# Kernel optimization log

Measured on AMD Instinct MI355X. Metric: run time of the kernel, lower is better.

The kernel has to match this reference:

```python
import jax, jax.numpy as jnp
import numpy as np

B, S, D = 1, 2048, 4096
H, KV = 32, 8
HD = D // H  # 128
NEG = -1e9


def _rope(t, cos, sin):
    # t: [B,S,h,HD]; cos/sin: [S,HD//2] -> broadcast [1,S,1,HD//2]
    tr = t[..., 0::2]
    ti = t[..., 1::2]
    c = cos[None, :, None, :]
    s = sin[None, :, None, :]
    out_r = tr * c - ti * s
    out_i = tr * s + ti * c
    # interleave back: (..., HD//2, 2) -> (..., HD)
    return jnp.stack([out_r, out_i], axis=-1).reshape(t.shape)


def setup_inputs() -> dict:
    key = jax.random.key(0)
    ks = jax.random.split(key, 5)
    w_scale = 0.02
    x = jax.random.normal(ks[0], (B, S, D), dtype=jnp.float32)
    wq = jax.random.normal(ks[1], (H * HD, D), dtype=jnp.float32) * w_scale
    wk = jax.random.normal(ks[2], (KV * HD, D), dtype=jnp.float32) * w_scale
    wv = jax.random.normal(ks[3], (KV * HD, D), dtype=jnp.float32) * w_scale
    wo = jax.random.normal(ks[4], (D, H * HD), dtype=jnp.float32) * w_scale
    # RoPE tables (theta = 10000)
    inv_freq = 1.0 / (10000.0 ** (np.arange(0, HD, 2, dtype=np.float32) / HD))
    angles = np.arange(S, dtype=np.float32)[:, None] * inv_freq[None, :]  # [S, HD//2]
    freqs_cos = jnp.asarray(np.cos(angles))
    freqs_sin = jnp.asarray(np.sin(angles))
    # causal additive mask [1,1,S,S]
    causal = jnp.tril(jnp.ones((S, S), dtype=bool))
    mask = jnp.where(causal, 0.0, NEG).astype(jnp.float32)[None, None]
    return {"x": x, "wq": wq, "wk": wk, "wv": wv, "wo": wo,
            "freqs_cos": freqs_cos, "freqs_sin": freqs_sin, "mask": mask}


def reference(x, wq, wk, wv, wo, freqs_cos, freqs_sin, mask):
    b, s, d = x.shape
    q = (x @ wq.T).reshape(b, s, H, HD)
    k = (x @ wk.T).reshape(b, s, KV, HD)
    v = (x @ wv.T).reshape(b, s, KV, HD)
    q = _rope(q, freqs_cos, freqs_sin)
    k = _rope(k, freqs_cos, freqs_sin)
    rep = H // KV
    k = jnp.repeat(k, rep, axis=2)  # [b,s,H,HD]
    v = jnp.repeat(v, rep, axis=2)
    scores = jnp.einsum('bshd,bthd->bhst', q, k) / jnp.sqrt(jnp.float32(HD))
    scores = scores + mask
    attn = jax.nn.softmax(scores, axis=-1)
    out = jnp.einsum('bhst,bthd->bshd', attn, v).reshape(b, s, H * HD)
    return out @ wo.T
```

## Files before the change

kernel.cpp:

```cpp
#include <hip/hip_runtime.h>
#include <hip/hip_bf16.h>
#include <math.h>

#define SEQ 2048
#define DIM 4096
#define NH 32
#define NKV 8
#define HD 128
#define KVD 1024
#define SCALE 0.08838834764831845f
#define NEGBIG -1000000000.0f

typedef __bf16 bf16;
typedef __attribute__((ext_vector_type(2))) __bf16 bf16x2;
typedef __attribute__((ext_vector_type(4))) __bf16 bf16x4;
typedef __attribute__((ext_vector_type(8))) __bf16 bf16x8;
typedef __attribute__((ext_vector_type(4))) float f32x4;

__device__ __forceinline__ void async_g2l16(const bf16* g, bf16* l) {
  __builtin_amdgcn_global_load_lds(
      (const __attribute__((address_space(1))) void*)g,
      (__attribute__((address_space(3))) void*)l,
      16, 0, 0);
}

#define SEG_X  2097152
#define SEG_WQ 4194304
#define SEG_WK 1048576
#define C0 SEG_X
#define C1 (C0 + SEG_WQ)
#define C2 (C1 + SEG_WK)
#define C3 (C2 + SEG_WK)
#define C4 (C3 + SEG_WQ)

__global__ void cast_all_kernel(const float* __restrict__ x,
                                const float* __restrict__ wq,
                                const float* __restrict__ wk,
                                const float* __restrict__ wv,
                                const float* __restrict__ wo,
                                bf16* __restrict__ xb, bf16* __restrict__ wqb,
                                bf16* __restrict__ wkb, bf16* __restrict__ wvb,
                                bf16* __restrict__ wob) {
  int i = blockIdx.x * 256 + threadIdx.x;
  const float* src; bf16* dst; int j;
  if (i < C0)      { src = x;  dst = xb;  j = i; }
  else if (i < C1) { src = wq; dst = wqb; j = i - C0; }
  else if (i < C2) { src = wk; dst = wkb; j = i - C1; }
  else if (i < C3) { src = wv; dst = wvb; j = i - C2; }
  else             { src = wo; dst = wob; j = i - C3; }
  float4 v = ((const float4*)src)[j];
  bf16x4 o;
  o[0] = (bf16)v.x; o[1] = (bf16)v.y; o[2] = (bf16)v.z; o[3] = (bf16)v.w;
  ((bf16x4*)dst)[j] = o;
}

__device__ __forceinline__ void gemm_core(
    const bf16* __restrict__ A, int lda,
    const bf16* __restrict__ B, int ldb,
    int K, int mBase, f32x4 acc[4][4])
{
  __shared__ __align__(16) bf16 As[128 * 32];
  __shared__ __align__(16) bf16 Bs[128 * 32];

  const int tid  = threadIdx.x;
  const int lane = tid & 63;
  const int w    = tid >> 6;
  const int l15  = lane & 15;
  const int quad = lane >> 4;
  const int wr   = (w >> 1) * 64;
  const int wc   = (w & 1) * 64;

  const int srow = lane >> 2;
  const int kswz = ((lane & 3) ^ ((srow >> 1) & 3)) * 8;
  const bf16* gA0 = A + (size_t)(mBase + w * 16 + srow) * lda + kswz;
  const bf16* gA1 = gA0 + (size_t)64 * lda;
  const bf16* gB0 = B + (size_t)(w * 16 + srow) * ldb + kswz;
  const bf16* gB1 = gB0 + (size_t)64 * ldb;
  bf16* lA0 = As + w * 512;
  bf16* lA1 = As + (w + 4) * 512;
  bf16* lB0 = Bs + w * 512;
  bf16* lB1 = Bs + (w + 4) * 512;

  const f32x4 vzero = {0.f, 0.f, 0.f, 0.f};
#pragma unroll
  for (int mi = 0; mi < 4; ++mi)
#pragma unroll
    for (int ni = 0; ni < 4; ++ni) acc[mi][ni] = vzero;

  const int rsw = ((l15 >> 1) & 3);

  for (int k0 = 0; k0 < K; k0 += 32) {
    __syncthreads();
    async_g2l16(gA0 + k0, lA0);
    async_g2l16(gA1 + k0, lA1);
    async_g2l16(gB0 + k0, lB0);
    async_g2l16(gB1 + k0, lB1);
    __syncthreads();

    bf16x8 a[4], b[4];
#pragma unroll
    for (int mi = 0; mi < 4; ++mi)
      a[mi] = *(const bf16x8*)(As + (wr + mi * 16 + l15) * 32 +
                               ((quad ^ rsw) * 8));
#pragma unroll
    for (int ni = 0; ni < 4; ++ni)
      b[ni] = *(const bf16x8*)(Bs + (wc + ni * 16 + l15) * 32 +
                               ((quad ^ rsw) * 8));
#pragma unroll
    for (int mi = 0; mi < 4; ++mi)
#pragma unroll
      for (int ni = 0; ni < 4; ++ni)
        acc[mi][ni] = __builtin_amdgcn_mfma_f32_16x16x32_bf16(
            a[mi], b[ni], acc[mi][ni], 0, 0, 0);
  }
}

__global__ __launch_bounds__(256, 2) void qkv_gemm_kernel(
    const bf16* __restrict__ xb, const bf16* __restrict__ wqb,
    const bf16* __restrict__ wkb, const bf16* __restrict__ wvb,
    const float* __restrict__ fc, const float* __restrict__ fs,
    bf16* __restrict__ Qb, bf16* __restrict__ Kb, bf16* __restrict__ Vt)
{
  const int nb = blockIdx.x;
  const int mBase = blockIdx.y * 128;
  const bf16* Bm;
  if (nb < 32)      Bm = wqb + (size_t)nb * 128 * DIM;
  else if (nb < 40) Bm = wkb + (size_t)(nb - 32) * 128 * DIM;
  else              Bm = wvb + (size_t)(nb - 40) * 128 * DIM;

  f32x4 acc[4][4];
  gemm_core(xb, DIM, Bm, DIM, DIM, mBase, acc);

  const int tid  = threadIdx.x;
  const int lane = tid & 63;
  const int w    = tid >> 6;
  const int l15  = lane & 15;
  const int quad = lane >> 4;
  const int wr   = (w >> 1) * 64;
  const int wc   = (w & 1) * 64;

  if (nb < 40) {
    const bool isQ = (nb < 32);
    bf16* dst = isQ ? (Qb + nb * HD) : (Kb + (nb - 32) * HD);
    const int ldd = isQ ? DIM : KVD;
    const float sc = isQ ? SCALE : 1.0f;
    const int odd = l15 & 1;
#pragma unroll
    for (int mi = 0; mi < 4; ++mi) {
#pragma unroll
      for (int ni = 0; ni < 4; ++ni) {
        int d = wc + ni * 16 + l15;
        int fidx = d >> 1;
#pragma unroll
        for (int r = 0; r < 4; ++r) {
          int s = mBase + wr + mi * 16 + quad * 4 + r;
          float v  = acc[mi][ni][r];
          float pv = __shfl_xor(v, 1, 64);
          float c  = fc[s * 64 + fidx];
          float sn = fs[s * 64 + fidx];
          float o  = odd ? (pv * sn + v * c) : (v * c - pv * sn);
          dst[(size_t)s * ldd + d] = (bf16)(o * sc);
        }
      }
    }
  } else {
    const int t = nb - 40;
#pragma unroll
    for (int mi = 0; mi < 4; ++mi) {
      int srow = mBase + wr + mi * 16 + quad * 4;
#pragma unroll
      for (int ni = 0; ni < 4; ++ni) {
        int d = wc + ni * 16 + l15;
        bf16x4 pv;
#pragma unroll
        for (int r = 0; r < 4; ++r) pv[r] = (bf16)acc[mi][ni][r];
        *(bf16x4*)(Vt + ((size_t)t * HD + d) * SEQ + srow) = pv;
      }
    }
  }
}

__global__ __launch_bounds__(256, 2) void out_gemm_kernel(
    const bf16* __restrict__ attnb, const bf16* __restrict__ wob,
    float* __restrict__ out)
{
  const int mBase = blockIdx.y * 128;
  f32x4 acc[4][4];
  gemm_core(attnb, DIM, wob + (size_t)blockIdx.x * 128 * DIM, DIM, DIM,
            mBase, acc);

  const int tid  = threadIdx.x;
  const int lane = tid & 63;
  const int w    = tid >> 6;
  const int l15  = lane & 15;
  const int quad = lane >> 4;
  const int wr   = (w >> 1) * 64;
  const int wc   = (w & 1) * 64;
#pragma unroll
  for (int mi = 0; mi < 4; ++mi) {
    int row = mBase + wr + mi * 16 + quad * 4;
#pragma unroll
    for (int ni = 0; ni < 4; ++ni) {
      int col = blockIdx.x * 128 + wc + ni * 16 + l15;
#pragma unroll
      for (int r = 0; r < 4; ++r)
        out[(size_t)(row + r) * DIM + col] = acc[mi][ni][r];
    }
  }
}

__global__ __launch_bounds__(256, 2) void attn_kernel(
    const bf16* __restrict__ Qb, const bf16* __restrict__ Kb,
    const bf16* __restrict__ Vt, bf16* __restrict__ attnb)
{
  __shared__ __align__(16) bf16 Ks[64 * 128];
  __shared__ __align__(16) bf16 Vs[128 * 64];
  __shared__ __align__(16) bf16 Ps[128 * 64];

  const int b    = blockIdx.x;
  const int half = b >> 8;
  const int r8   = b & 255;
  const int h    = (half << 4) | (r8 >> 4);
  const int qt   = half ? (r8 & 15) : 15 - (r8 & 15);
  const int kvh  = h >> 2;
  const int qbase = qt * 128;

  const int tid  = threadIdx.x;
  const int lane = tid & 63;
  const int w    = tid >> 6;
  const int l15  = lane & 15;
  const int quad = lane >> 4;

  bf16x8 qfrag[2][4];
#pragma unroll
  for (int n = 0; n < 2; ++n) {
    int q = qbase + w * 32 + n * 16 + l15;
#pragma unroll
    for (int ks = 0; ks < 4; ++ks)
      qfrag[n][ks] = *(const bf16x8*)(Qb + (size_t)q * DIM + h * HD +
                                      ks * 32 + quad * 8);
  }

  const f32x4 vzero = {0.f, 0.f, 0.f, 0.f};
  f32x4 oacc[8][2];
#pragma unroll
  for (int dm = 0; dm < 8; ++dm)
#pragma unroll
    for (int n = 0; n < 2; ++n) oacc[dm][n] = vzero;
  float m_run[2] = {-1e30f, -1e30f};
  float l_run[2] = {0.f, 0.f};

  const int nkt = 2 * (qt + 1);
  for (int kt = 0; kt < nkt; ++kt) {
    const int kbase = kt * 64;

    __syncthreads();
#pragma unroll
    for (int t = 0; t < 4; ++t) {
      int kr0 = w * 16 + t * 4;
      int krow = kr0 + (lane >> 4);
      int kg = (lane & 15) ^ (krow & 7);
      async_g2l16(Kb + (size_t)(kbase + krow) * KVD + kvh * HD + kg * 8,
                  Ks + kr0 * 128);
      int vr0 = w * 32 + t * 8;
      int d = vr0 + (lane >> 3);
      int vg = (lane & 7) ^ (d & 7);
      async_g2l16(Vt + ((size_t)kvh * HD + d) * SEQ + kbase + vg * 8,
                  Vs + vr0 * 64);
    }
    __syncthreads();

    f32x4 sacc[4][2];
#pragma unroll
    for (int kg = 0; kg < 4; ++kg)
#pragma unroll
      for (int n = 0; n < 2; ++n) sacc[kg][n] = vzero;
#pragma unroll
    for (int kg = 0; kg < 4; ++kg) {
      bf16x8 kf[4];
#pragma unroll
      for (int ks = 0; ks < 4; ++ks) {
        int row = kg * 16 + l15;
        kf[ks] = *(const bf16x8*)(Ks + row * 128 +
                                  (((ks * 4 + quad) ^ (row & 7)) * 8));
      }
#pragma unroll
      for (int n = 0; n < 2; ++n)
#pragma unroll
        for (int ks = 0; ks < 4; ++ks)
          sacc[kg][n] = __builtin_amdgcn_mfma_f32_16x16x32_bf16(
              kf[ks], qfrag[n][ks], sacc[kg][n], 0, 0, 0);
    }

#pragma unroll
    for (int n = 0; n < 2; ++n) {
      const int qloc = w * 32 + n * 16 + l15;
      const int qglob = qbase + qloc;
      if (kbase + 63 > qbase + w * 32 + n * 16) {
#pragma unroll
        for (int kg = 0; kg < 4; ++kg)
#pragma unroll
          for (int r = 0; r < 4; ++r) {
            int key = kbase + kg * 16 + quad * 4 + r;
            if (key > qglob) sacc[kg][n][r] = NEGBIG;
          }
      }
      float mx = -1e30f;
#pragma unroll
      for (int kg = 0; kg < 4; ++kg)
#pragma unroll
        for (int r = 0; r < 4; ++r) mx = fmaxf(mx, sacc[kg][n][r]);
      mx = fmaxf(mx, __shfl_xor(mx, 16, 64));
      mx = fmaxf(mx, __shfl_xor(mx, 32, 64));
      float mnew = fmaxf(m_run[n], mx);
      float alpha = __expf(m_run[n] - mnew);
      m_run[n] = mnew;
      float rs = 0.f;
#pragma unroll
      for (int kg = 0; kg < 4; ++kg) {
        bf16x4 pk;
#pragma unroll
        for (int r = 0; r < 4; ++r) {
          float p = __expf(sacc[kg][n][r] - mnew);
          rs += p;
          pk[r] = (bf16)p;
        }
        int g16 = (kg * 2 + (quad >> 1)) ^ (qloc & 7);
        *(bf16x4*)(Ps + qloc * 64 + g16 * 8 + (quad & 1) * 4) = pk;
      }
      rs += __shfl_xor(rs, 16, 64);
      rs += __shfl_xor(rs, 32, 64);
      l_run[n] = alpha * l_run[n] + rs;
#pragma unroll
      for (int dm = 0; dm < 8; ++dm)
#pragma unroll
        for (int r = 0; r < 4; ++r) oacc[dm][n][r] *= alpha;
    }

    bf16x8 pf[2][2];
#pragma unroll
    for (int kk = 0; kk < 2; ++kk)
#pragma unroll
      for (int n = 0; n < 2; ++n) {
        int qloc = w * 32 + n * 16 + l15;
        pf[kk][n] = *(const bf16x8*)(Ps + qloc * 64 +
                                     (((kk * 4 + quad) ^ (qloc & 7)) * 8));
      }
#pragma unroll
    for (int dm = 0; dm < 8; ++dm) {
#pragma unroll
      for (int kk = 0; kk < 2; ++kk) {
        int d = dm * 16 + l15;
        bf16x8 vf = *(const bf16x8*)(Vs + d * 64 +
                                     (((kk * 4 + quad) ^ (d & 7)) * 8));
#pragma unroll
        for (int n = 0; n < 2; ++n)
          oacc[dm][n] = __builtin_amdgcn_mfma_f32_16x16x32_bf16(
              vf, pf[kk][n], oacc[dm][n], 0, 0, 0);
      }
    }
  }

#pragma unroll
  for (int n = 0; n < 2; ++n) {
    float inv = 1.0f / l_run[n];
    int q = qbase + w * 32 + n * 16 + l15;
#pragma unroll
    for (int dm = 0; dm < 8; ++dm) {
      bf16x4 ov;
#pragma unroll
      for (int r = 0; r < 4; ++r) ov[r] = (bf16)(oacc[dm][n][r] * inv);
      *(bf16x4*)(attnb + (size_t)q * DIM + h * HD + dm * 16 + quad * 4) = ov;
    }
  }
}

extern "C" void kernel_launch(void* const* d_in, const int* in_sizes, int n_in,
                              void* d_out, int out_size, void* d_ws, size_t ws_size,
                              hipStream_t stream) {
  const float* x  = (const float*)d_in[0];
  const float* wq = (const float*)d_in[1];
  const float* wk = (const float*)d_in[2];
  const float* wv = (const float*)d_in[3];
  const float* wo = (const float*)d_in[4];
  const float* fc = (const float*)d_in[5];
  const float* fs = (const float*)d_in[6];
  float* out = (float*)d_out;

  size_t off = 0;
  char* wsb = (char*)d_ws;
  auto take = [&](size_t bytes) -> void* {
    void* p = wsb + off;
    off += (bytes + 255) & ~(size_t)255;
    return p;
  };
  bf16*  xb    = (bf16*)take((size_t)SEQ * DIM * 2);
  bf16*  wqb   = (bf16*)take((size_t)DIM * DIM * 2);
  bf16*  wkb   = (bf16*)take((size_t)KVD * DIM * 2);
  bf16*  wvb   = (bf16*)take((size_t)KVD * DIM * 2);
  bf16*  wob   = (bf16*)take((size_t)DIM * DIM * 2);
  bf16*  Qb    = (bf16*)take((size_t)SEQ * DIM * 2);
  bf16*  Kb    = (bf16*)take((size_t)SEQ * KVD * 2);
  bf16*  Vt    = (bf16*)take((size_t)NKV * HD * SEQ * 2);
  bf16*  attnb = (bf16*)take((size_t)SEQ * DIM * 2);

  cast_all_kernel<<<C4 / 256, 256, 0, stream>>>(x, wq, wk, wv, wo,
                                                xb, wqb, wkb, wvb, wob);

  qkv_gemm_kernel<<<dim3(48, 16), 256, 0, stream>>>(xb, wqb, wkb, wvb,
                                                    fc, fs, Qb, Kb, Vt);

  attn_kernel<<<dim3(512), 256, 0, stream>>>(Qb, Kb, Vt, attnb);

  out_gemm_kernel<<<dim3(32, 16), 256, 0, stream>>>(attnb, wob, out);
}
```

Before: 483.1 us.

## Fuse fp32-to-bf16 casting into GEMM tile loads and drop cast kernel

Removes the standalone cast kernel and has the QKV and output GEMMs load fp32 activations and weights directly into shared memory via async global-to-LDS copies, converting to bf16 when fragments are read from LDS. This removes a full pass that wrote and re-read bf16 copies of all weights and the input. In exchange, each GEMM tile load moves twice the bytes, LDS footprint grows, and conversion instructions are added inside the inner loop, which may reduce occupancy or stall the MFMA pipeline.

```diff
diff --git a/kernel.cpp b/kernel.cpp
--- a/kernel.cpp
+++ b/kernel.cpp
@@ -17,50 +17,22 @@
 typedef __attribute__((ext_vector_type(8))) __bf16 bf16x8;
 typedef __attribute__((ext_vector_type(4))) float f32x4;
 
-__device__ __forceinline__ void async_g2l16(const bf16* g, bf16* l) {
+__device__ __forceinline__ void async_g2l16(const void* g, void* l) {
   __builtin_amdgcn_global_load_lds(
       (const __attribute__((address_space(1))) void*)g,
       (__attribute__((address_space(3))) void*)l,
       16, 0, 0);
 }
 
-#define SEG_X  2097152
-#define SEG_WQ 4194304
-#define SEG_WK 1048576
-#define C0 SEG_X
-#define C1 (C0 + SEG_WQ)
-#define C2 (C1 + SEG_WK)
-#define C3 (C2 + SEG_WK)
-#define C4 (C3 + SEG_WQ)
-
-__global__ void cast_all_kernel(const float* __restrict__ x,
-                                const float* __restrict__ wq,
-                                const float* __restrict__ wk,
-                                const float* __restrict__ wv,
-                                const float* __restrict__ wo,
-                                bf16* __restrict__ xb, bf16* __restrict__ wqb,
-                                bf16* __restrict__ wkb, bf16* __restrict__ wvb,
-                                bf16* __restrict__ wob) {
-  int i = blockIdx.x * 256 + threadIdx.x;
-  const float* src; bf16* dst; int j;
-  if (i < C0)      { src = x;  dst = xb;  j = i; }
-  else if (i < C1) { src = wq; dst = wqb; j = i - C0; }
-  else if (i < C2) { src = wk; dst = wkb; j = i - C1; }
-  else if (i < C3) { src = wv; dst = wvb; j = i - C2; }
-  else             { src = wo; dst = wob; j = i - C3; }
-  float4 v = ((const float4*)src)[j];
-  bf16x4 o;
-  o[0] = (bf16)v.x; o[1] = (bf16)v.y; o[2] = (bf16)v.z; o[3] = (bf16)v.w;
-  ((bf16x4*)dst)[j] = o;
-}
-
+template<typename TA>
 __device__ __forceinline__ void gemm_core(
-    const bf16* __restrict__ A, int lda,
-    const bf16* __restrict__ B, int ldb,
+    const TA* __restrict__ A, int lda,
+    const float* __restrict__ B, int ldb,
     int K, int mBase, f32x4 acc[4][4])
 {
-  __shared__ __align__(16) bf16 As[128 * 32];
-  __shared__ __align__(16) bf16 Bs[128 * 32];
+  constexpr bool AF32 = (sizeof(TA) == 4);
+  __shared__ __align__(16) TA    As[128 * 32];
+  __shared__ __align__(16) float Bs[128 * 32];
 
   const int tid  = threadIdx.x;
   const int lane = tid & 63;
@@ -70,16 +42,11 @@
   const int wr   = (w >> 1) * 64;
   const int wc   = (w & 1) * 64;
 
+  const int r8 = lane >> 3;
+  const int gsw = (lane & 7) ^ r8;
+
   const int srow = lane >> 2;
   const int kswz = ((lane & 3) ^ ((srow >> 1) & 3)) * 8;
-  const bf16* gA0 = A + (size_t)(mBase + w * 16 + srow) * lda + kswz;
-  const bf16* gA1 = gA0 + (size_t)64 * lda;
-  const bf16* gB0 = B + (size_t)(w * 16 + srow) * ldb + kswz;
-  const bf16* gB1 = gB0 + (size_t)64 * ldb;
-  bf16* lA0 = As + w * 512;
-  bf16* lA1 = As + (w + 4) * 512;
-  bf16* lB0 = Bs + w * 512;
-  bf16* lB1 = Bs + (w + 4) * 512;
 
   const f32x4 vzero = {0.f, 0.f, 0.f, 0.f};
 #pragma unroll
@@ -91,21 +58,56 @@
 
   for (int k0 = 0; k0 < K; k0 += 32) {
     __syncthreads();
-    async_g2l16(gA0 + k0, lA0);
-    async_g2l16(gA1 + k0, lA1);
-    async_g2l16(gB0 + k0, lB0);
-    async_g2l16(gB1 + k0, lB1);
+    if constexpr (AF32) {
+#pragma unroll
+      for (int t = 0; t < 4; ++t) {
+        int row = w * 32 + t * 8 + r8;
+        async_g2l16((const float*)A + (size_t)(mBase + row) * lda + k0 + gsw * 4,
+                    As + (w * 32 + t * 8) * 32);
+      }
+    } else {
+      async_g2l16((const bf16*)A + (size_t)(mBase + w * 16 + srow) * lda + k0 + kswz,
+                  As + w * 512);
+      async_g2l16((const bf16*)A + (size_t)(mBase + 64 + w * 16 + srow) * lda + k0 + kswz,
+                  As + (w + 4) * 512);
+    }
+#pragma unroll
+    for (int t = 0; t < 4; ++t) {
+      int row = w * 32 + t * 8 + r8;
+      async_g2l16(B + (size_t)row * ldb + k0 + gsw * 4,
+                  Bs + (w * 32 + t * 8) * 32);
+    }
     __syncthreads();
 
     bf16x8 a[4], b[4];
 #pragma unroll
-    for (int mi = 0; mi < 4; ++mi)
-      a[mi] = *(const bf16x8*)(As + (wr + mi * 16 + l15) * 32 +
-                               ((quad ^ rsw) * 8));
-#pragma unroll
-    for (int ni = 0; ni < 4; ++ni)
-      b[ni] = *(const bf16x8*)(Bs + (wc + ni * 16 + l15) * 32 +
-                               ((quad ^ rsw) * 8));
+    for (int mi = 0; mi < 4; ++mi) {
+      int row = wr + mi * 16 + l15;
+      if constexpr (AF32) {
+        const float* rp = (const float*)As + row * 32;
+        int p0 = (2 * quad) ^ (row & 7);
+        f32x4 lo = *(const f32x4*)(rp + p0 * 4);
+        f32x4 hi = *(const f32x4*)(rp + (p0 ^ 1) * 4);
+        bf16x8 f;
+#pragma unroll
+        for (int j = 0; j < 4; ++j) { f[j] = (bf16)lo[j]; f[4 + j] = (bf16)hi[j]; }
+        a[mi] = f;
+      } else {
+        a[mi] = *(const bf16x8*)((const bf16*)As + row * 32 + ((quad ^ rsw) * 8));
+      }
+    }
+#pragma unroll
+    for (int ni = 0; ni < 4; ++ni) {
+      int row = wc + ni * 16 + l15;
+      const float* rp = Bs + row * 32;
+      int p0 = (2 * quad) ^ (row & 7);
+      f32x4 lo = *(const f32x4*)(rp + p0 * 4);
+      f32x4 hi = *(const f32x4*)(rp + (p0 ^ 1) * 4);
+      bf16x8 f;
+#pragma unroll
+      for (int j = 0; j < 4; ++j) { f[j] = (bf16)lo[j]; f[4 + j] = (bf16)hi[j]; }
+      b[ni] = f;
+    }
 #pragma unroll
     for (int mi = 0; mi < 4; ++mi)
 #pragma unroll
@@ -116,20 +118,20 @@
 }
 
 __global__ __launch_bounds__(256, 2) void qkv_gemm_kernel(
-    const bf16* __restrict__ xb, const bf16* __restrict__ wqb,
-    const bf16* __restrict__ wkb, const bf16* __restrict__ wvb,
+    const float* __restrict__ x, const float* __restrict__ wq,
+    const float* __restrict__ wk, const float* __restrict__ wv,
     const float* __restrict__ fc, const float* __restrict__ fs,
     bf16* __restrict__ Qb, bf16* __restrict__ Kb, bf16* __restrict__ Vt)
 {
   const int nb = blockIdx.x;
   const int mBase = blockIdx.y * 128;
-  const bf16* Bm;
-  if (nb < 32)      Bm = wqb + (size_t)nb * 128 * DIM;
-  else if (nb < 40) Bm = wkb + (size_t)(nb - 32) * 128 * DIM;
-  else              Bm = wvb + (size_t)(nb - 40) * 128 * DIM;
+  const float* Bm;
+  if (nb < 32)      Bm = wq + (size_t)nb * 128 * DIM;
+  else if (nb < 40) Bm = wk + (size_t)(nb - 32) * 128 * DIM;
+  else              Bm = wv + (size_t)(nb - 40) * 128 * DIM;
 
   f32x4 acc[4][4];
-  gemm_core(xb, DIM, Bm, DIM, DIM, mBase, acc);
+  gemm_core<float>(x, DIM, Bm, DIM, DIM, mBase, acc);
 
   const int tid  = threadIdx.x;
   const int lane = tid & 63;
@@ -181,13 +183,13 @@
 }
 
 __global__ __launch_bounds__(256, 2) void out_gemm_kernel(
-    const bf16* __restrict__ attnb, const bf16* __restrict__ wob,
+    const bf16* __restrict__ attnb, const float* __restrict__ wo,
     float* __restrict__ out)
 {
   const int mBase = blockIdx.y * 128;
   f32x4 acc[4][4];
-  gemm_core(attnb, DIM, wob + (size_t)blockIdx.x * 128 * DIM, DIM, DIM,
-            mBase, acc);
+  gemm_core<bf16>(attnb, DIM, wo + (size_t)blockIdx.x * 128 * DIM, DIM, DIM,
+                  mBase, acc);
 
   const int tid  = threadIdx.x;
   const int lane = tid & 63;
@@ -394,23 +396,15 @@
     off += (bytes + 255) & ~(size_t)255;
     return p;
   };
-  bf16*  xb    = (bf16*)take((size_t)SEQ * DIM * 2);
-  bf16*  wqb   = (bf16*)take((size_t)DIM * DIM * 2);
-  bf16*  wkb   = (bf16*)take((size_t)KVD * DIM * 2);
-  bf16*  wvb   = (bf16*)take((size_t)KVD * DIM * 2);
-  bf16*  wob   = (bf16*)take((size_t)DIM * DIM * 2);
   bf16*  Qb    = (bf16*)take((size_t)SEQ * DIM * 2);
   bf16*  Kb    = (bf16*)take((size_t)SEQ * KVD * 2);
   bf16*  Vt    = (bf16*)take((size_t)NKV * HD * SEQ * 2);
   bf16*  attnb = (bf16*)take((size_t)SEQ * DIM * 2);
 
-  cast_all_kernel<<<C4 / 256, 256, 0, stream>>>(x, wq, wk, wv, wo,
-                                                xb, wqb, wkb, wvb, wob);
-
-  qkv_gemm_kernel<<<dim3(48, 16), 256, 0, stream>>>(xb, wqb, wkb, wvb,
+  qkv_gemm_kernel<<<dim3(48, 16), 256, 0, stream>>>(x, wq, wk, wv,
                                                     fc, fs, Qb, Kb, Vt);
 
   attn_kernel<<<dim3(512), 256, 0, stream>>>(Qb, Kb, Vt, attnb);
 
-  out_gemm_kernel<<<dim3(32, 16), 256, 0, stream>>>(attnb, wob, out);
-}
+  out_gemm_kernel<<<dim3(32, 16), 256, 0, stream>>>(attnb, wo, out);
+}
```

Measured after the change: 573.6 us. +18.7%, slower.

## Shrink attention query tile to 64 rows and double grid size

Applied to the files above, without the earlier changes.

The attention kernel now gives each block 64 query rows instead of 128, with each wave owning 16 rows, and launches 1024 blocks instead of 512. Causal masking is applied only on the diagonal key tile, and the P buffer in shared memory is halved. Launch bounds rise to 3 blocks per CU. The aim is more parallelism, better load balance across CUs and higher occupancy through fewer registers per thread. In exchange, each K/V tile loaded into shared memory is reused by half as many queries, so K/V traffic roughly doubles.

```diff
diff --git a/kernel.cpp b/kernel.cpp
--- a/kernel.cpp
+++ b/kernel.cpp
@@ -17,7 +17,7 @@
 typedef __attribute__((ext_vector_type(8))) __bf16 bf16x8;
 typedef __attribute__((ext_vector_type(4))) float f32x4;
 
-__device__ __forceinline__ void async_g2l16(const bf16* g, bf16* l) {
+__device__ __forceinline__ void async_g2l16(const void* g, void* l) {
   __builtin_amdgcn_global_load_lds(
       (const __attribute__((address_space(1))) void*)g,
       (__attribute__((address_space(3))) void*)l,
@@ -209,48 +209,43 @@
   }
 }
 
-__global__ __launch_bounds__(256, 2) void attn_kernel(
+__global__ __launch_bounds__(256, 3) void attn_kernel(
     const bf16* __restrict__ Qb, const bf16* __restrict__ Kb,
     const bf16* __restrict__ Vt, bf16* __restrict__ attnb)
 {
   __shared__ __align__(16) bf16 Ks[64 * 128];
   __shared__ __align__(16) bf16 Vs[128 * 64];
-  __shared__ __align__(16) bf16 Ps[128 * 64];
+  __shared__ __align__(16) bf16 Ps[64 * 64];
 
   const int b    = blockIdx.x;
-  const int half = b >> 8;
-  const int r8   = b & 255;
-  const int h    = (half << 4) | (r8 >> 4);
-  const int qt   = half ? (r8 & 15) : 15 - (r8 & 15);
+  const int half = b >> 9;
+  const int r    = b & 511;
+  const int h    = (half << 4) | (r >> 5);
+  const int qt   = half ? (r & 31) : 31 - (r & 31);
   const int kvh  = h >> 2;
-  const int qbase = qt * 128;
+  const int qbase = qt * 64;
 
   const int tid  = threadIdx.x;
   const int lane = tid & 63;
   const int w    = tid >> 6;
   const int l15  = lane & 15;
   const int quad = lane >> 4;
-
-  bf16x8 qfrag[2][4];
-#pragma unroll
-  for (int n = 0; n < 2; ++n) {
-    int q = qbase + w * 32 + n * 16 + l15;
-#pragma unroll
-    for (int ks = 0; ks < 4; ++ks)
-      qfrag[n][ks] = *(const bf16x8*)(Qb + (size_t)q * DIM + h * HD +
-                                      ks * 32 + quad * 8);
-  }
+  const int qloc = w * 16 + l15;
+  const int qglob = qbase + qloc;
+
+  bf16x8 qfrag[4];
+#pragma unroll
+  for (int ks = 0; ks < 4; ++ks)
+    qfrag[ks] = *(const bf16x8*)(Qb + (size_t)qglob * DIM + h * HD +
+                                 ks * 32 + quad * 8);
 
   const f32x4 vzero = {0.f, 0.f, 0.f, 0.f};
-  f32x4 oacc[8][2];
-#pragma unroll
-  for (int dm = 0; dm < 8; ++dm)
-#pragma unroll
-    for (int n = 0; n < 2; ++n) oacc[dm][n] = vzero;
-  float m_run[2] = {-1e30f, -1e30f};
-  float l_run[2] = {0.f, 0.f};
-
-  const int nkt = 2 * (qt + 1);
+  f32x4 oacc[8];
+#pragma unroll
+  for (int dm = 0; dm < 8; ++dm) oacc[dm] = vzero;
+  float m_run = -1e30f, l_run = 0.f;
+
+  const int nkt = qt + 1;
   for (int kt = 0; kt < nkt; ++kt) {
     const int kbase = kt * 64;
 
@@ -270,11 +265,9 @@
     }
     __syncthreads();
 
-    f32x4 sacc[4][2];
-#pragma unroll
-    for (int kg = 0; kg < 4; ++kg)
-#pragma unroll
-      for (int n = 0; n < 2; ++n) sacc[kg][n] = vzero;
+    f32x4 sacc[4];
+#pragma unroll
+    for (int kg = 0; kg < 4; ++kg) sacc[kg] = vzero;
 #pragma unroll
     for (int kg = 0; kg < 4; ++kg) {
       bf16x8 kf[4];
@@ -285,67 +278,57 @@
                                   (((ks * 4 + quad) ^ (row & 7)) * 8));
       }
 #pragma unroll
-      for (int n = 0; n < 2; ++n)
-#pragma unroll
-        for (int ks = 0; ks < 4; ++ks)
-          sacc[kg][n] = __builtin_amdgcn_mfma_f32_16x16x32_bf16(
-              kf[ks], qfrag[n][ks], sacc[kg][n], 0, 0, 0);
-    }
-
-#pragma unroll
-    for (int n = 0; n < 2; ++n) {
-      const int qloc = w * 32 + n * 16 + l15;
-      const int qglob = qbase + qloc;
-      if (kbase + 63 > qbase + w * 32 + n * 16) {
-#pragma unroll
-        for (int kg = 0; kg < 4; ++kg)
-#pragma unroll
-          for (int r = 0; r < 4; ++r) {
-            int key = kbase + kg * 16 + quad * 4 + r;
-            if (key > qglob) sacc[kg][n][r] = NEGBIG;
-          }
-      }
-      float mx = -1e30f;
+      for (int ks = 0; ks < 4; ++ks)
+        sacc[kg] = __builtin_amdgcn_mfma_f32_16x16x32_bf16(
+            kf[ks], qfrag[ks], sacc[kg], 0, 0, 0);
+    }
+
+    if (kt == qt) {
 #pragma unroll
       for (int kg = 0; kg < 4; ++kg)
 #pragma unroll
-        for (int r = 0; r < 4; ++r) mx = fmaxf(mx, sacc[kg][n][r]);
-      mx = fmaxf(mx, __shfl_xor(mx, 16, 64));
-      mx = fmaxf(mx, __shfl_xor(mx, 32, 64));
-      float mnew = fmaxf(m_run[n], mx);
-      float alpha = __expf(m_run[n] - mnew);
-      m_run[n] = mnew;
-      float rs = 0.f;
-#pragma unroll
-      for (int kg = 0; kg < 4; ++kg) {
-        bf16x4 pk;
-#pragma unroll
         for (int r = 0; r < 4; ++r) {
-          float p = __expf(sacc[kg][n][r] - mnew);
-          rs += p;
-          pk[r] = (bf16)p;
+          int key = kbase + kg * 16 + quad * 4 + r;
+          if (key > qglob) sacc[kg][r] = NEGBIG;
         }
-        int g16 = (kg * 2 + (quad >> 1)) ^ (qloc & 7);
-        *(bf16x4*)(Ps + qloc * 64 + g16 * 8 + (quad & 1) * 4) = pk;
-      }
-      rs += __shfl_xor(rs, 16, 64);
-      rs += __shfl_xor(rs, 32, 64);
-      l_run[n] = alpha * l_run[n] + rs;
-#pragma unroll
-      for (int dm = 0; dm < 8; ++dm)
-#pragma unroll
-        for (int r = 0; r < 4; ++r) oacc[dm][n][r] *= alpha;
-    }
-
-    bf16x8 pf[2][2];
+    }
+
+    float mx = -1e30f;
+#pragma unroll
+    for (int kg = 0; kg < 4; ++kg)
+#pragma unroll
+      for (int r = 0; r < 4; ++r) mx = fmaxf(mx, sacc[kg][r]);
+    mx = fmaxf(mx, __shfl_xor(mx, 16, 64));
+    mx = fmaxf(mx, __shfl_xor(mx, 32, 64));
+    float mnew = fmaxf(m_run, mx);
+    float alpha = __expf(m_run - mnew);
+    m_run = mnew;
+    float rs = 0.f;
+#pragma unroll
+    for (int kg = 0; kg < 4; ++kg) {
+      bf16x4 pk;
+#pragma unroll
+      for (int r = 0; r < 4; ++r) {
+        float p = __expf(sacc[kg][r] - mnew);
+        rs += p;
+        pk[r] = (bf16)p;
+      }
+      int g16 = (kg * 2 + (quad >> 1)) ^ (qloc & 7);
+      *(bf16x4*)(Ps + qloc * 64 + g16 * 8 + (quad & 1) * 4) = pk;
+    }
+    rs += __shfl_xor(rs, 16, 64);
+    rs += __shfl_xor(rs, 32, 64);
+    l_run = alpha * l_run + rs;
+#pragma unroll
+    for (int dm = 0; dm < 8; ++dm)
+#pragma unroll
+      for (int r = 0; r < 4; ++r) oacc[dm][r] *= alpha;
+
+    bf16x8 pf[2];
 #pragma unroll
     for (int kk = 0; kk < 2; ++kk)
-#pragma unroll
-      for (int n = 0; n < 2; ++n) {
-        int qloc = w * 32 + n * 16 + l15;
-        pf[kk][n] = *(const bf16x8*)(Ps + qloc * 64 +
-                                     (((kk * 4 + quad) ^ (qloc & 7)) * 8));
-      }
+      pf[kk] = *(const bf16x8*)(Ps + qloc * 64 +
+                                (((kk * 4 + quad) ^ (qloc & 7)) * 8));
 #pragma unroll
     for (int dm = 0; dm < 8; ++dm) {
 #pragma unroll
@@ -353,24 +336,20 @@
         int d = dm * 16 + l15;
         bf16x8 vf = *(const bf16x8*)(Vs + d * 64 +
                                      (((kk * 4 + quad) ^ (d & 7)) * 8));
-#pragma unroll
-        for (int n = 0; n < 2; ++n)
-          oacc[dm][n] = __builtin_amdgcn_mfma_f32_16x16x32_bf16(
-              vf, pf[kk][n], oacc[dm][n], 0, 0, 0);
-      }
-    }
-  }
-
-#pragma unroll
-  for (int n = 0; n < 2; ++n) {
-    float inv = 1.0f / l_run[n];
-    int q = qbase + w * 32 + n * 16 + l15;
+        oacc[dm] = __builtin_amdgcn_mfma_f32_16x16x32_bf16(
+            vf, pf[kk], oacc[dm], 0, 0, 0);
+      }
+    }
+  }
+
+  {
+    float inv = 1.0f / l_run;
 #pragma unroll
     for (int dm = 0; dm < 8; ++dm) {
       bf16x4 ov;
 #pragma unroll
-      for (int r = 0; r < 4; ++r) ov[r] = (bf16)(oacc[dm][n][r] * inv);
-      *(bf16x4*)(attnb + (size_t)q * DIM + h * HD + dm * 16 + quad * 4) = ov;
+      for (int r = 0; r < 4; ++r) ov[r] = (bf16)(oacc[dm][r] * inv);
+      *(bf16x4*)(attnb + (size_t)qglob * DIM + h * HD + dm * 16 + quad * 4) = ov;
     }
   }
 }
@@ -410,7 +389,7 @@
   qkv_gemm_kernel<<<dim3(48, 16), 256, 0, stream>>>(xb, wqb, wkb, wvb,
                                                     fc, fs, Qb, Kb, Vt);
 
-  attn_kernel<<<dim3(512), 256, 0, stream>>>(Qb, Kb, Vt, attnb);
+  attn_kernel<<<dim3(1024), 256, 0, stream>>>(Qb, Kb, Vt, attnb);
 
   out_gemm_kernel<<<dim3(32, 16), 256, 0, stream>>>(attnb, wob, out);
 }
```

Result: slower. 499.8 us (+3.5%).
